# Performance work log

Measured on AMD Instinct MI355X. Metric: run time of the kernel, lower is better.

The kernel has to match this reference:

```python
import jax, jax.numpy as jnp
import numpy as np
import math

B, NX, NY = 4, 64, 64
IN_DIM, OUT_DIM = 3, 3
DIM, DEPTH, HEADS, DH, FF_MULT = 192, 6, 8, 64, 4
INNER = HEADS * DH              # 512
FF = DIM * FF_MULT              # 768
M = int(DH * math.log(DH))      # 266 random features (performer default)
GROUPS = 8
LATENT_STEPS = 1
EPS_SN, EPS_K, EPS_GN = 1e-5, 1e-4, 1e-5


def setup_inputs() -> dict:
    rng = np.random.default_rng(0)
    f = lambda *s: jnp.asarray(rng.standard_normal(s).astype(np.float32) * 0.02)
    # unitary forward operator (SVD-whitened in torch == orthogonal matrix)
    Q, _ = np.linalg.qr(rng.standard_normal((DIM, DIM)).astype(np.float32))
    return {
        "x": jnp.asarray(rng.standard_normal((B, NX, NY, IN_DIM)).astype(np.float32)),
        "to_in_w": f(DIM, IN_DIM), "to_in_b": f(DIM),
        "pos_emb": f(1, NX * NY, DIM),
        "proj": jnp.asarray(rng.standard_normal((DEPTH, M, DH)).astype(np.float32)),
        "sn_attn_g": jnp.ones((DEPTH,), jnp.float32),
        "wq": f(DEPTH, INNER, DIM), "wk": f(DEPTH, INNER, DIM), "wv": f(DEPTH, INNER, DIM),
        "wo": f(DEPTH, DIM, INNER), "bo": f(DEPTH, DIM),
        "sn_ff_g": jnp.ones((DEPTH,), jnp.float32),
        "w1": f(DEPTH, FF, DIM), "b1": f(DEPTH, FF),
        "w2": f(DEPTH, DIM, FF), "b2": f(DEPTH, DIM),
        "expand_w": f(DIM, DIM),
        "fwd_w": jnp.asarray(Q.astype(np.float32)),
        "dec_lin_w": f(DIM, DIM), "dec_lin_b": f(DIM),
        "gn_g": jnp.ones((DIM,), jnp.float32), "gn_b": jnp.zeros((DIM,), jnp.float32),
        "c9_w": f(DIM, DIM // GROUPS, 9, 9), "c9_b": f(DIM),
        "c7_w": f(DIM // 2, DIM // GROUPS, 7, 7), "c7_b": f(DIM // 2),
        "c5_w": f(DIM // 4, (DIM // 2) // GROUPS, 5, 5), "c5_b": f(DIM // 4),
        "c1_w": f(OUT_DIM, DIM // 4, 1, 1), "c1_b": f(OUT_DIM),
        "latent_steps": LATENT_STEPS,
    }


def _scalenorm(x, g):
    n = jnp.linalg.norm(x, axis=-1, keepdims=True) * (x.shape[-1] ** -0.5)
    return x / jnp.maximum(n, EPS_SN) * g


def _softmax_features(data, proj, is_query):
    # data: [b,h,n,d]; proj: [m,d] -> FAVOR+ softmax-kernel features [b,h,n,m]
    dn = data.shape[-1] ** -0.25
    ratio = proj.shape[0] ** -0.5
    dd = jnp.einsum('bhnd,md->bhnm', data * dn, proj)
    diag = 0.5 * jnp.sum(data * data, -1) * (dn * dn)  # [b,h,n]
    if is_query:
        mx = jnp.max(dd, axis=-1, keepdims=True)
    else:
        mx = jnp.max(dd, axis=(-1, -2), keepdims=True)
    return ratio * (jnp.exp(dd - diag[..., None] - mx) + EPS_K)


def _attn(x, proj, wq, wk, wv, wo, bo):
    b, n, _ = x.shape
    split = lambda t: t.reshape(b, n, HEADS, DH).transpose(0, 2, 1, 3)
    q = split(x @ wq.T); k = split(x @ wk.T); v = split(x @ wv.T)
    qp = _softmax_features(q, proj, True)
    kp = _softmax_features(k, proj, False)
    context = jnp.einsum('bhnm,bhnd->bhmd', kp, v)            # [b,h,m,d]
    denom = jnp.einsum('bhnm,bhm->bhn', qp, kp.sum(2))
    out = jnp.einsum('bhnm,bhmd->bhnd', qp, context) / denom[..., None]
    out = out.transpose(0, 2, 1, 3).reshape(b, n, INNER)
    return out @ wo.T + bo


def _circ_conv(x, w, b, groups):
    p = w.shape[-1] // 2
    x = jnp.pad(x, ((0, 0), (0, 0), (p, p), (p, p)), mode='wrap')
    y = jax.lax.conv_general_dilated(x, w, (1, 1), 'VALID',
        dimension_numbers=('NCHW', 'OIHW', 'NCHW'), feature_group_count=groups)
    return y + b[None, :, None, None]


def _group_norm(x, g, b):
    B_, C, H, W = x.shape
    xg = x.reshape(B_, GROUPS, C // GROUPS, H, W)
    mu = xg.mean((2, 3, 4), keepdims=True)
    var = xg.var((2, 3, 4), keepdims=True)
    xn = ((xg - mu) * jax.lax.rsqrt(var + EPS_GN)).reshape(B_, C, H, W)
    return xn * g[None, :, None, None] + b[None, :, None, None]


def reference(x, to_in_w, to_in_b, pos_emb, proj, sn_attn_g, wq, wk, wv, wo, bo,
              sn_ff_g, w1, b1, w2, b2, expand_w, fwd_w, dec_lin_w, dec_lin_b,
              gn_g, gn_b, c9_w, c9_b, c7_w, c7_b, c5_w, c5_b, c1_w, c1_b, latent_steps):
    b, nx, ny, _ = x.shape
    h = x @ to_in_w.T + to_in_b                       # [b,nx,ny,dim]
    h = h.reshape(b, nx * ny, DIM) + pos_emb[:, :nx * ny]
    for i in range(DEPTH):                             # Performer: prenorm attn + prenorm FF
        h = h + _attn(_scalenorm(h, sn_attn_g[i]), proj[i], wq[i], wk[i], wv[i], wo[i], bo[i])
        hn = _scalenorm(h, sn_ff_g[i])
        h = h + (jax.nn.gelu(hn @ w1[i].T + b1[i], approximate=False) @ w2[i].T + b2[i])
    h = h.reshape(b, nx, ny, DIM) @ expand_w.T        # expand_latent (no bias)
    u, us = h, []
    for _ in range(latent_steps):
        u = u @ fwd_w.T                               # unitary forward operator
        us.append(u)
    u = jnp.concatenate(us, 0)                        # [(b*t), nx, ny, c]
    y = u @ dec_lin_w.T + dec_lin_b
    y = y.transpose(0, 3, 1, 2)                       # NCHW
    y = _group_norm(y, gn_g, gn_b)
    y = jax.nn.gelu(_circ_conv(y, c9_w, c9_b, GROUPS), approximate=False)
    y = jax.nn.gelu(_circ_conv(y, c7_w, c7_b, GROUPS), approximate=False)
    y = jax.nn.gelu(_circ_conv(y, c5_w, c5_b, GROUPS), approximate=False)
    y = jax.lax.conv_general_dilated(y, c1_w, (1, 1), 'VALID',
        dimension_numbers=('NCHW', 'OIHW', 'NCHW')) + c1_b[None, :, None, None]
    # einops '(b t) c nx ny -> b t nx ny c'
    y = y.reshape(b, latent_steps, OUT_DIM, nx, ny).transpose(0, 1, 3, 4, 2)
    return y
```

## Files before the change

### kernel.cpp

```cpp
#include <hip/hip_runtime.h>
#include <cmath>

#define NB      4
#define NTOK    4096
#define BNTOK   16384
#define CDIM    192
#define CINNER  512
#define NHEADS  8
#define DHEAD   64
#define CFF     768
#define MFEAT   266
#define NDEPTH  6

#define DN      0.35355339059327373f
#define RATIO   0.06131393394849658f

typedef unsigned short u16;
typedef __attribute__((ext_vector_type(8))) short s16x8;
typedef __attribute__((ext_vector_type(8))) u16  u16x8;
typedef __attribute__((ext_vector_type(4))) float f32x4;

#define OFF_H    0ull
#define OFF_HN   3145728ull
#define OFF_Q    6291456ull
#define OFF_K    14680064ull
#define OFF_V    23068672ull
#define OFF_BIG  31457280ull
#define OFF_PJ   44040192ull
#define OFF_CTXT 44163072ull
#define OFF_KMAX 47368192ull
#define OFF_GNP  47368448ull
#define OFF_GNS  47369472ull
#define OFF_WHI  47370240ull
#define OFF_WLO  49489920ull
#define WOFF_QKV 0ull
#define WOFF_WO  1769472ull
#define WOFF_W1  2359296ull
#define WOFF_W2  3244032ull
#define WOFF_EXP 4128768ull
#define WOFF_FWD 4165632ull
#define WOFF_DEC 4202496ull

#define PJL      20480
#define CTXTN    819200

__device__ __forceinline__ float gelu_f(float x) {
    return 0.5f * x * (1.0f + erff(x * 0.7071067811865476f));
}
__device__ __forceinline__ unsigned f2ord(float f) {
    int i = __float_as_int(f);
    return (i >= 0) ? ((unsigned)i | 0x80000000u) : (unsigned)(~i);
}
__device__ __forceinline__ float ord2f(unsigned u) {
    int i = (u & 0x80000000u) ? (int)(u & 0x7fffffffu) : ~(int)u;
    return __int_as_float(i);
}
__device__ __forceinline__ void split_bf16(float a, u16& h, u16& l) {
    unsigned ua = __float_as_uint(a);
    unsigned rh = (ua + 0x7FFFu + ((ua >> 16) & 1u)) >> 16;
    h = (u16)rh;
    float hf = __uint_as_float(rh << 16);
    float lo = a - hf;
    unsigned ul = __float_as_uint(lo);
    unsigned rl = (ul + 0x7FFFu + ((ul >> 16) & 1u)) >> 16;
    l = (u16)rl;
}
__device__ __forceinline__ u16 hi_bf16(float a) {
    unsigned ua = __float_as_uint(a);
    return (u16)((ua + 0x7FFFu + ((ua >> 16) & 1u)) >> 16);
}

__global__ __launch_bounds__(256) void cvt_qkv(const float* __restrict__ wq,
    const float* __restrict__ wk, const float* __restrict__ wv,
    u16* __restrict__ hi, u16* __restrict__ lo)
{
    int idx = blockIdx.x * 256 + threadIdx.x;
    int l = idx / 294912, rem = idx - l * 294912;
    int r = rem / 192, c = rem - r * 192;
    float v;
    if (r < 512)       v = wq[((size_t)l * 512 + r) * 192 + c];
    else if (r < 1024) v = wk[((size_t)l * 512 + (r - 512)) * 192 + c];
    else               v = wv[((size_t)l * 512 + (r - 1024)) * 192 + c];
    u16 h, lw; split_bf16(v, h, lw);
    hi[idx] = h; lo[idx] = lw;
}

__global__ __launch_bounds__(256) void cvt_w(const float* __restrict__ src,
    u16* __restrict__ hi, u16* __restrict__ lo, int n)
{
    int idx = blockIdx.x * 256 + threadIdx.x;
    if (idx < n) {
        u16 h, l; split_bf16(src[idx], h, l);
        hi[idx] = h; lo[idx] = l;
    }
}

__global__ __launch_bounds__(256) void cvt_dec(const float* __restrict__ e,
    const float* __restrict__ f, const float* __restrict__ d,
    u16* __restrict__ hi, u16* __restrict__ lo)
{
    int idx = blockIdx.x * 256 + threadIdx.x;
    if (idx >= 110592) return;
    int which = idx / 36864, rem = idx - which * 36864;
    float v = (which == 0) ? e[rem] : (which == 1) ? f[rem] : d[rem];
    u16 h, l; split_bf16(v, h, l);
    hi[idx] = h; lo[idx] = l;
}

__global__ __launch_bounds__(256) void cvt_pj(const float* __restrict__ proj,
    u16* __restrict__ hi, u16* __restrict__ lo)
{
    int idx = blockIdx.x * 256 + threadIdx.x;
    int l = idx / PJL, rem = idx - l * PJL;
    int m = rem >> 6, k = rem & 63;
    float v = (m < MFEAT) ? proj[(size_t)l * MFEAT * DHEAD + m * 64 + k] : 0.f;
    u16 h, lw; split_bf16(v, h, lw);
    hi[idx] = h; lo[idx] = lw;
}

__global__ __launch_bounds__(256) void input_embed(const float* __restrict__ x,
    const float* __restrict__ w, const float* __restrict__ bvec,
    const float* __restrict__ pos, float* __restrict__ h)
{
    int idx = blockIdx.x * 256 + threadIdx.x;
    int row = idx / CDIM, c = idx - row * CDIM;
    int p = row & (NTOK - 1);
    const float* xr = x + (size_t)row * 3;
    h[idx] = xr[0]*w[c*3+0] + xr[1]*w[c*3+1] + xr[2]*w[c*3+2] + bvec[c] + pos[(size_t)p*CDIM + c];
}

__global__ __launch_bounds__(256) void scalenorm_kernel(const float* __restrict__ in,
    float* __restrict__ out, const float* __restrict__ gptr, int gidx)
{
    int wv = threadIdx.x >> 6, lane = threadIdx.x & 63;
    int row = blockIdx.x * 4 + wv;
    const float* p = in + (size_t)row * CDIM;
    float x0 = p[lane], x1 = p[lane + 64], x2 = p[lane + 128];
    float ss = x0*x0 + x1*x1 + x2*x2;
    #pragma unroll
    for (int off = 32; off; off >>= 1) ss += __shfl_xor(ss, off);
    float g = gptr[gidx];
    float n = sqrtf(ss * (1.0f / 192.0f));
    float s = g / fmaxf(n, 1e-5f);
    float* o = out + (size_t)row * CDIM;
    o[lane] = x0 * s; o[lane + 64] = x1 * s; o[lane + 128] = x2 * s;
}

#define LP 40
__global__ __launch_bounds__(256) void gemm_mfma(const float* __restrict__ A,
    const u16* __restrict__ Bhi, const u16* __restrict__ Blo,
    const float* __restrict__ bias, const float* __restrict__ resid,
    float* __restrict__ C, int M, int N, int K, int epi)
{
    __shared__ u16 a_hi[128 * LP], a_lo[128 * LP], b_hi[128 * LP], b_lo[128 * LP];
    const int tid = threadIdx.x;
    const int n0 = blockIdx.x * 128, m0 = blockIdx.y * 128;
    const int wave = tid >> 6, lane = tid & 63;
    const int wr = wave >> 1, wc = wave & 1;
    const int fr = lane & 15, q = lane >> 4;
    f32x4 acc[4][4];
    #pragma unroll
    for (int i = 0; i < 4; ++i)
        #pragma unroll
        for (int j = 0; j < 4; ++j) { acc[i][j][0]=0.f; acc[i][j][1]=0.f; acc[i][j][2]=0.f; acc[i][j][3]=0.f; }

    const int srow = tid >> 1, sc0 = (tid & 1) * 16;
    const float* aptr = A + (size_t)(m0 + srow) * K + sc0;
    const bool bval = (n0 + srow) < N;
    const u16* bhp = Bhi + (size_t)(n0 + srow) * K + sc0;
    const u16* blp = Blo + (size_t)(n0 + srow) * K + sc0;
    const int soff = srow * LP + sc0;
    const int aoffb = (wr * 64 + fr) * LP + q * 8;
    const int boffb = (wc * 64 + fr) * LP + q * 8;

    for (int kc = 0; kc < K; kc += 32) {
        float4 f0 = *(const float4*)(aptr + kc);
        float4 f1 = *(const float4*)(aptr + kc + 4);
        float4 f2 = *(const float4*)(aptr + kc + 8);
        float4 f3 = *(const float4*)(aptr + kc + 12);
        u16x8 h0, l0, h1, l1;
        {
            float v[16] = {f0.x,f0.y,f0.z,f0.w, f1.x,f1.y,f1.z,f1.w,
                           f2.x,f2.y,f2.z,f2.w, f3.x,f3.y,f3.z,f3.w};
            u16 hh[16], ll[16];
            #pragma unroll
            for (int i = 0; i < 16; ++i) split_bf16(v[i], hh[i], ll[i]);
            #pragma unroll
            for (int i = 0; i < 8; ++i) { h0[i]=hh[i]; l0[i]=ll[i]; h1[i]=hh[8+i]; l1[i]=ll[8+i]; }
        }
        *(u16x8*)&a_hi[soff]     = h0;  *(u16x8*)&a_hi[soff + 8] = h1;
        *(u16x8*)&a_lo[soff]     = l0;  *(u16x8*)&a_lo[soff + 8] = l1;
        u16x8 bh0 = (u16x8)0, bh1 = (u16x8)0, bl0 = (u16x8)0, bl1 = (u16x8)0;
        if (bval) {
            bh0 = *(const u16x8*)(bhp + kc);  bh1 = *(const u16x8*)(bhp + kc + 8);
            bl0 = *(const u16x8*)(blp + kc);  bl1 = *(const u16x8*)(blp + kc + 8);
        }
        *(u16x8*)&b_hi[soff]     = bh0;  *(u16x8*)&b_hi[soff + 8] = bh1;
        *(u16x8*)&b_lo[soff]     = bl0;  *(u16x8*)&b_lo[soff + 8] = bl1;
        __syncthreads();
        s16x8 Ah[4], Al[4], Bh[4], Bl[4];
        #pragma unroll
        for (int t = 0; t < 4; ++t) {
            Ah[t] = *(const s16x8*)&a_hi[aoffb + t * 16 * LP];
            Al[t] = *(const s16x8*)&a_lo[aoffb + t * 16 * LP];
            Bh[t] = *(const s16x8*)&b_hi[boffb + t * 16 * LP];
            Bl[t] = *(const s16x8*)&b_lo[boffb + t * 16 * LP];
        }
        #pragma unroll
        for (int i = 0; i < 4; ++i)
            #pragma unroll
            for (int j = 0; j < 4; ++j)
                acc[i][j] = __builtin_amdgcn_mfma_f32_16x16x32_bf16(Ah[i], Bh[j], acc[i][j], 0, 0, 0);
        #pragma unroll
        for (int i = 0; i < 4; ++i)
            #pragma unroll
            for (int j = 0; j < 4; ++j)
                acc[i][j] = __builtin_amdgcn_mfma_f32_16x16x32_bf16(Ah[i], Bl[j], acc[i][j], 0, 0, 0);
        #pragma unroll
        for (int i = 0; i < 4; ++i)
            #pragma unroll
            for (int j = 0; j < 4; ++j)
                acc[i][j] = __builtin_amdgcn_mfma_f32_16x16x32_bf16(Al[i], Bh[j], acc[i][j], 0, 0, 0);
        __syncthreads();
    }
    const int c0 = n0 + wc * 64;
    const int rowb = m0 + wr * 64;
    #pragma unroll
    for (int j = 0; j < 4; ++j) {
        int c = c0 + j * 16 + fr;
        if (c >= N) continue;
        float bb = (epi & 1) ? bias[c] : 0.f;
        float* cp;
        if (epi & 8) cp = C + (size_t)(c >> 9) * 8388608ull + (size_t)(c & 511);
        else         cp = C + c;
        const float* rp = (epi & 4) ? (resid + c) : nullptr;
        #pragma unroll
        for (int i = 0; i < 4; ++i) {
            #pragma unroll
            for (int r = 0; r < 4; ++r) {
                int row = rowb + i * 16 + q * 4 + r;
                float val = acc[i][j][r] + bb;
                if (epi & 2) val = gelu_f(val);
                if (epi & 4) val += rp[(size_t)row * N];
                size_t off = (epi & 8) ? (size_t)row * 512 : (size_t)row * N;
                cp[off] = val;
            }
        }
    }
}

__global__ void kmax_init(unsigned* kmaxu) {
    if (threadIdx.x < NDEPTH * 32) kmaxu[threadIdx.x] = 0u;
}

__global__ __launch_bounds__(256) void kmax2_kernel(const float* __restrict__ Km,
    const u16* __restrict__ pjh, unsigned* __restrict__ kmaxu)
{
    __shared__ __align__(16) u16 khi[64 * 72];
    __shared__ float wred[4];
    const int tid = threadIdx.x;
    const int nt = blockIdx.x, bh = blockIdx.y;
    const int b = bh >> 3, hh = bh & 7;
    const int wave = tid >> 6, lane = tid & 63;
    const int fr = lane & 15, quad = lane >> 4;
    float lm = -1e30f;
    const size_t kbase = ((size_t)b * NTOK) * CINNER + hh * DHEAD;
    for (int ch = 0; ch < 8; ++ch) {
        const int n0 = nt * 512 + ch * 64;
        __syncthreads();
        {
            int tok = tid >> 2, koff = (tid & 3) * 16;
            const float* kp = Km + kbase + (size_t)(n0 + tok) * CINNER + koff;
            u16 hh16[16];
            #pragma unroll
            for (int qd = 0; qd < 4; ++qd) {
                float4 f = *(const float4*)(kp + qd * 4);
                hh16[qd*4+0] = hi_bf16(f.x * DN); hh16[qd*4+1] = hi_bf16(f.y * DN);
                hh16[qd*4+2] = hi_bf16(f.z * DN); hh16[qd*4+3] = hi_bf16(f.w * DN);
            }
            u16x8 v0, v1;
            #pragma unroll
            for (int i = 0; i < 8; ++i) { v0[i] = hh16[i]; v1[i] = hh16[8+i]; }
            *(u16x8*)&khi[tok * 72 + koff] = v0;
            *(u16x8*)&khi[tok * 72 + koff + 8] = v1;
        }
        __syncthreads();
        int rowA = (wave * 16 + fr) * 72;
        s16x8 A0 = *(const s16x8*)&khi[rowA + quad * 8];
        s16x8 A1 = *(const s16x8*)&khi[rowA + 32 + quad * 8];
        for (int ct = 0; ct < 17; ++ct) {
            const u16* bp = pjh + (ct * 16 + fr) * 64 + quad * 8;
            s16x8 B0 = *(const s16x8*)bp;
            s16x8 B1 = *(const s16x8*)(bp + 32);
            f32x4 t; t[0]=0.f; t[1]=0.f; t[2]=0.f; t[3]=0.f;
            t = __builtin_amdgcn_mfma_f32_16x16x32_bf16(A0, B0, t, 0, 0, 0);
            t = __builtin_amdgcn_mfma_f32_16x16x32_bf16(A1, B1, t, 0, 0, 0);
            if (ct * 16 + fr < MFEAT) {
                #pragma unroll
                for (int r = 0; r < 4; ++r) lm = fmaxf(lm, t[r]);
            }
        }
    }
    #pragma unroll
    for (int off = 32; off; off >>= 1) lm = fmaxf(lm, __shfl_xor(lm, off));
    if (lane == 0) wred[wave] = lm;
    __syncthreads();
    if (tid == 0) {
        float m = fmaxf(fmaxf(wred[0], wred[1]), fmaxf(wred[2], wred[3]));
        atomicMax(kmaxu + bh, f2ord(m));
    }
}

__global__ __launch_bounds__(256) void ctx2_kernel(const float* __restrict__ Km,
    const float* __restrict__ Vm, const u16* __restrict__ pjh, const u16* __restrict__ pjl,
    const unsigned* __restrict__ kmaxu, float* __restrict__ part)
{
    __shared__ __align__(16) u16 khi[32 * 72], klo[32 * 72];
    __shared__ __align__(16) u16 vth[80 * 40], vtl[80 * 40];
    __shared__ __align__(16) u16 kph[64 * 40], kpl[64 * 40];
    __shared__ float diag[32];
    const int tid = threadIdx.x;
    const int bh = blockIdx.x, seg = blockIdx.y;
    const int b = bh >> 3, hh = bh & 7;
    const int wave = tid >> 6, lane = tid & 63;
    const int fr = lane & 15, quad = lane >> 4;
    const float kmx = ord2f(kmaxu[bh]);
    for (int i = tid; i < 16 * 40; i += 256) {
        int row = 64 + i / 40, col = i - (i / 40) * 40;
        vth[row * 40 + col] = (row == 64) ? (u16)0x3F80 : (u16)0;
        vtl[row * 40 + col] = 0;
    }
    f32x4 accv[5][5];
    #pragma unroll
    for (int i = 0; i < 5; ++i)
        #pragma unroll
        for (int j = 0; j < 5; ++j) { accv[i][j][0]=0.f; accv[i][j][1]=0.f; accv[i][j][2]=0.f; accv[i][j][3]=0.f; }
    const size_t rowbase = ((size_t)b * NTOK) * CINNER + hh * DHEAD;
    const int rt = wave & 1, ctp = wave >> 1;
    for (int nc = 0; nc < 16; ++nc) {
        const int n0 = seg * 512 + nc * 32;
        __syncthreads();
        {
            int tok = tid >> 3, koff = (tid & 7) * 8;
            const float* kp = Km + rowbase + (size_t)(n0 + tok) * CINNER + koff;
            float4 f0 = *(const float4*)kp;
            float4 f1 = *(const float4*)(kp + 4);
            float v[8] = {f0.x*DN, f0.y*DN, f0.z*DN, f0.w*DN, f1.x*DN, f1.y*DN, f1.z*DN, f1.w*DN};
            u16x8 hv, lv; float ps = 0.f;
            #pragma unroll
            for (int i = 0; i < 8; ++i) { u16 h, l; split_bf16(v[i], h, l); hv[i]=h; lv[i]=l; ps += v[i]*v[i]; }
            *(u16x8*)&khi[tok * 72 + koff] = hv;
            *(u16x8*)&klo[tok * 72 + koff] = lv;
            ps += __shfl_xor(ps, 1); ps += __shfl_xor(ps, 2); ps += __shfl_xor(ps, 4);
            if ((tid & 7) == 0) diag[tok] = 0.5f * ps;
            const float* vp = Vm + rowbase + (size_t)(n0 + tok) * CINNER + koff;
            float4 g0 = *(const float4*)vp;
            float4 g1 = *(const float4*)(vp + 4);
            float vv[8] = {g0.x, g0.y, g0.z, g0.w, g1.x, g1.y, g1.z, g1.w};
            #pragma unroll
            for (int i = 0; i < 8; ++i) {
                u16 h, l; split_bf16(vv[i], h, l);
                vth[(koff + i) * 40 + tok] = h;
                vtl[(koff + i) * 40 + tok] = l;
            }
        }
        __syncthreads();
        for (int mc = 0; mc < 5; ++mc) {
            f32x4 dd2[2];
            dd2[0][0]=0.f; dd2[0][1]=0.f; dd2[0][2]=0.f; dd2[0][3]=0.f;
            dd2[1] = dd2[0];
            {
                int rowA = (rt * 16 + fr) * 72;
                s16x8 A0h = *(const s16x8*)&khi[rowA + quad * 8];
                s16x8 A1h = *(const s16x8*)&khi[rowA + 32 + quad * 8];
                s16x8 A0l = *(const s16x8*)&klo[rowA + quad * 8];
                s16x8 A1l = *(const s16x8*)&klo[rowA + 32 + quad * 8];
                #pragma unroll
                for (int c = 0; c < 2; ++c) {
                    int ct = mc * 4 + ctp * 2 + c;
                    const u16* bph = pjh + (ct * 16 + fr) * 64 + quad * 8;
                    const u16* bpl = pjl + (ct * 16 + fr) * 64 + quad * 8;
                    s16x8 B0h = *(const s16x8*)bph, B1h = *(const s16x8*)(bph + 32);
                    s16x8 B0l = *(const s16x8*)bpl, B1l = *(const s16x8*)(bpl + 32);
                    dd2[c] = __builtin_amdgcn_mfma_f32_16x16x32_bf16(A0h, B0h, dd2[c], 0, 0, 0);
                    dd2[c] = __builtin_amdgcn_mfma_f32_16x16x32_bf16(A0h, B0l, dd2[c], 0, 0, 0);
                    dd2[c] = __builtin_amdgcn_mfma_f32_16x16x32_bf16(A0l, B0h, dd2[c], 0, 0, 0);
                    dd2[c] = __builtin_amdgcn_mfma_f32_16x16x32_bf16(A1h, B1h, dd2[c], 0, 0, 0);
                    dd2[c] = __builtin_amdgcn_mfma_f32_16x16x32_bf16(A1h, B1l, dd2[c], 0, 0, 0);
                    dd2[c] = __builtin_amdgcn_mfma_f32_16x16x32_bf16(A1l, B1h, dd2[c], 0, 0, 0);
                }
            }
            #pragma unroll
            for (int c = 0; c < 2; ++c) {
                int ct = mc * 4 + ctp * 2 + c;
                bool valid = (ct * 16 + fr) < MFEAT;
                ushort4 ph, pl;
                #pragma unroll
                for (int r = 0; r < 4; ++r) {
                    float dgv = diag[rt * 16 + quad * 4 + r];
                    float val = valid ? RATIO * (expf(dd2[c][r] - dgv - kmx) + 1e-4f) : 0.f;
                    u16 h, l; split_bf16(val, h, l);
                    (&ph.x)[r] = h; (&pl.x)[r] = l;
                }
                int ml = (ctp * 2 + c) * 16 + fr;
                *(ushort4*)&kph[ml * 40 + rt * 16 + quad * 4] = ph;
                *(ushort4*)&kpl[ml * 40 + rt * 16 + quad * 4] = pl;
            }
            __syncthreads();
            {
                s16x8 Bh = *(const s16x8*)&kph[(wave * 16 + fr) * 40 + quad * 8];
                s16x8 Bl = *(const s16x8*)&kpl[(wave * 16 + fr) * 40 + quad * 8];
                #pragma unroll
                for (int rt2 = 0; rt2 < 5; ++rt2) {
                    s16x8 Ah = *(const s16x8*)&vth[(rt2 * 16 + fr) * 40 + quad * 8];
                    s16x8 Al = *(const s16x8*)&vtl[(rt2 * 16 + fr) * 40 + quad * 8];
                    accv[rt2][mc] = __builtin_amdgcn_mfma_f32_16x16x32_bf16(Ah, Bh, accv[rt2][mc], 0, 0, 0);
                    accv[rt2][mc] = __builtin_amdgcn_mfma_f32_16x16x32_bf16(Ah, Bl, accv[rt2][mc], 0, 0, 0);
                    accv[rt2][mc] = __builtin_amdgcn_mfma_f32_16x16x32_bf16(Al, Bh, accv[rt2][mc], 0, 0, 0);
                }
            }
            __syncthreads();
        }
    }
    float* pb = part + ((size_t)(seg * 32 + bh)) * 80 * 320;
    #pragma unroll
    for (int rt2 = 0; rt2 < 5; ++rt2) {
        #pragma unroll
        for (int mc = 0; mc < 5; ++mc) {
            int ct = mc * 4 + wave;
            #pragma unroll
            for (int r = 0; r < 4; ++r)
                pb[(size_t)(rt2 * 16 + quad * 4 + r) * 320 + ct * 16 + fr] = accv[rt2][mc][r];
        }
    }
}

__global__ __launch_bounds__(256) void ctxt_reduce(const float* __restrict__ part,
    u16* __restrict__ cth, u16* __restrict__ ctl)
{
    int idx = blockIdx.x * 256 + threadIdx.x;
    float s = 0.f;
    #pragma unroll
    for (int sg = 0; sg < 8; ++sg) s += part[(size_t)sg * CTXTN + idx];
    u16 h, l; split_bf16(s, h, l);
    cth[idx] = h; ctl[idx] = l;
}

__global__ __launch_bounds__(256) void qside2_kernel(const float* __restrict__ Qm,
    const u16* __restrict__ pjh, const u16* __restrict__ pjl,
    const u16* __restrict__ cth, const u16* __restrict__ ctl,
    float* __restrict__ attn_out)
{
    __shared__ __align__(16) u16 qhi[64 * 72], qlo[64 * 72];
    __shared__ __align__(16) u16 slabh[4][16 * 72], slabl[4][16 * 72];
    __shared__ float diag[64];
    const int tid = threadIdx.x;
    const int nt = blockIdx.x, bh = blockIdx.y;
    const int b = bh >> 3, hh = bh & 7;
    const int wave = tid >> 6, lane = tid & 63;
    const int fr = lane & 15, quad = lane >> 4;
    const int n0 = nt * 64;
    {
        int tok = tid >> 2, koff = (tid & 3) * 16;
        const float* qp = Qm + ((size_t)(b * NTOK + n0 + tok)) * CINNER + hh * DHEAD + koff;
        float v[16]; float ps = 0.f;
        #pragma unroll
        for (int qd = 0; qd < 4; ++qd) {
            float4 f = *(const float4*)(qp + qd * 4);
            v[qd*4+0]=f.x*DN; v[qd*4+1]=f.y*DN; v[qd*4+2]=f.z*DN; v[qd*4+3]=f.w*DN;
        }
        u16x8 h0, l0, h1, l1;
        #pragma unroll
        for (int i = 0; i < 8; ++i) {
            u16 h, l; split_bf16(v[i], h, l); h0[i]=h; l0[i]=l;
            split_bf16(v[8+i], h, l); h1[i]=h; l1[i]=l;
        }
        #pragma unroll
        for (int i = 0; i < 16; ++i) ps += v[i]*v[i];
        *(u16x8*)&qhi[tok * 72 + koff] = h0;  *(u16x8*)&qhi[tok * 72 + koff + 8] = h1;
        *(u16x8*)&qlo[tok * 72 + koff] = l0;  *(u16x8*)&qlo[tok * 72 + koff + 8] = l1;
        ps += __shfl_xor(ps, 1); ps += __shfl_xor(ps, 2);
        if ((tid & 3) == 0) diag[tok] = 0.5f * ps;
    }
    __syncthreads();
    f32x4 dd[20];
    #pragma unroll
    for (int ct = 0; ct < 20; ++ct) { dd[ct][0]=0.f; dd[ct][1]=0.f; dd[ct][2]=0.f; dd[ct][3]=0.f; }
    {
        int rowA = (wave * 16 + fr) * 72;
        s16x8 A0h = *(const s16x8*)&qhi[rowA + quad * 8];
        s16x8 A1h = *(const s16x8*)&qhi[rowA + 32 + quad * 8];
        s16x8 A0l = *(const s16x8*)&qlo[rowA + quad * 8];
        s16x8 A1l = *(const s16x8*)&qlo[rowA + 32 + quad * 8];
        #pragma unroll
        for (int ct = 0; ct < 20; ++ct) {
            const u16* bph = pjh + (ct * 16 + fr) * 64 + quad * 8;
            const u16* bpl = pjl + (ct * 16 + fr) * 64 + quad * 8;
            s16x8 B0h = *(const s16x8*)bph, B1h = *(const s16x8*)(bph + 32);
            s16x8 B0l = *(const s16x8*)bpl, B1l = *(const s16x8*)(bpl + 32);
            dd[ct] = __builtin_amdgcn_mfma_f32_16x16x32_bf16(A0h, B0h, dd[ct], 0, 0, 0);
            dd[ct] = __builtin_amdgcn_mfma_f32_16x16x32_bf16(A0h, B0l, dd[ct], 0, 0, 0);
            dd[ct] = __builtin_amdgcn_mfma_f32_16x16x32_bf16(A0l, B0h, dd[ct], 0, 0, 0);
            dd[ct] = __builtin_amdgcn_mfma_f32_16x16x32_bf16(A1h, B1h, dd[ct], 0, 0, 0);
            dd[ct] = __builtin_amdgcn_mfma_f32_16x16x32_bf16(A1h, B1l, dd[ct], 0, 0, 0);
            dd[ct] = __builtin_amdgcn_mfma_f32_16x16x32_bf16(A1l, B1h, dd[ct], 0, 0, 0);
        }
    }
    float pm[4] = {-1e30f, -1e30f, -1e30f, -1e30f};
    #pragma unroll
    for (int ct = 0; ct < 20; ++ct) {
        if (ct * 16 + fr < MFEAT) {
            #pragma unroll
            for (int r = 0; r < 4; ++r) pm[r] = fmaxf(pm[r], dd[ct][r]);
        }
    }
    #pragma unroll
    for (int r = 0; r < 4; ++r) {
        pm[r] = fmaxf(pm[r], __shfl_xor(pm[r], 1));
        pm[r] = fmaxf(pm[r], __shfl_xor(pm[r], 2));
        pm[r] = fmaxf(pm[r], __shfl_xor(pm[r], 4));
        pm[r] = fmaxf(pm[r], __shfl_xor(pm[r], 8));
    }
    float dg[4];
    #pragma unroll
    for (int r = 0; r < 4; ++r) dg[r] = diag[wave * 16 + quad * 4 + r];
    #pragma unroll
    for (int ct = 0; ct < 20; ++ct) {
        bool valid = (ct * 16 + fr) < MFEAT;
        #pragma unroll
        for (int r = 0; r < 4; ++r)
            dd[ct][r] = valid ? RATIO * (expf(dd[ct][r] - dg[r] - pm[r]) + 1e-4f) : 0.f;
    }
    f32x4 acc[5];
    #pragma unroll
    for (int dt = 0; dt < 5; ++dt) { acc[dt][0]=0.f; acc[dt][1]=0.f; acc[dt][2]=0.f; acc[dt][3]=0.f; }
    u16* sh = slabh[wave];  u16* sl = slabl[wave];
    for (int mc = 0; mc < 5; ++mc) {
        #pragma unroll
        for (int c = 0; c < 4; ++c) {
            int ct = mc * 4 + c;
            #pragma unroll
            for (int r = 0; r < 4; ++r) {
                u16 h, l; split_bf16(dd[ct][r], h, l);
                int tok = quad * 4 + r;
                sh[tok * 72 + c * 16 + fr] = h;
                sl[tok * 72 + c * 16 + fr] = l;
            }
        }
        __syncthreads();
        #pragma unroll
        for (int ks = 0; ks < 2; ++ks) {
            s16x8 Ah = *(const s16x8*)&sh[fr * 72 + ks * 32 + quad * 8];
            s16x8 Al = *(const s16x8*)&sl[fr * 72 + ks * 32 + quad * 8];
            #pragma unroll
            for (int dt = 0; dt < 5; ++dt) {
                const u16* bph = cth + ((size_t)bh * 80 + dt * 16 + fr) * 320 + mc * 64 + ks * 32 + quad * 8;
                const u16* bpl = ctl + ((size_t)bh * 80 + dt * 16 + fr) * 320 + mc * 64 + ks * 32 + quad * 8;
                s16x8 Bh = *(const s16x8*)bph;
                s16x8 Bl = *(const s16x8*)bpl;
                acc[dt] = __builtin_amdgcn_mfma_f32_16x16x32_bf16(Ah, Bh, acc[dt], 0, 0, 0);
                acc[dt] = __builtin_amdgcn_mfma_f32_16x16x32_bf16(Ah, Bl, acc[dt], 0, 0, 0);
                acc[dt] = __builtin_amdgcn_mfma_f32_16x16x32_bf16(Al, Bh, acc[dt], 0, 0, 0);
            }
        }
        __syncthreads();
    }
    #pragma unroll
    for (int r = 0; r < 4; ++r) {
        float denom = __shfl(acc[4][r], lane & 48);
        float inv = 1.0f / denom;
        int token = n0 + wave * 16 + quad * 4 + r;
        float* op = attn_out + ((size_t)(b * NTOK + token)) * CINNER + hh * DHEAD;
        #pragma unroll
        for (int dt = 0; dt < 4; ++dt)
            op[dt * 16 + fr] = acc[dt][r] * inv;
    }
}

__global__ __launch_bounds__(256) void gn_part_kernel(const float* __restrict__ y,
    float2* __restrict__ part)
{
    __shared__ float s_s[256], s_q[256];
    const int tid = threadIdx.x;
    const int sp = blockIdx.x, g = blockIdx.y, b = blockIdx.z;
    int p = sp * 256 + tid;
    const float* base = y + ((size_t)(b * NTOK + p)) * CDIM + g * 24;
    float s = 0.f, q = 0.f;
    #pragma unroll
    for (int i = 0; i < 24; ++i) { float v = base[i]; s += v; q += v * v; }
    s_s[tid] = s; s_q[tid] = q;
    __syncthreads();
    for (int st = 128; st; st >>= 1) {
        if (tid < st) { s_s[tid] += s_s[tid + st]; s_q[tid] += s_q[tid + st]; }
        __syncthreads();
    }
    if (tid == 0) part[(b * 8 + g) * 16 + sp] = make_float2(s_s[0], s_q[0]);
}

__global__ void gn_stat_kernel(const float2* __restrict__ part, float2* __restrict__ stat)
{
    int bg = threadIdx.x;
    if (bg < 32) {
        float s = 0.f, q = 0.f;
        for (int i = 0; i < 16; ++i) { float2 v = part[bg * 16 + i]; s += v.x; q += v.y; }
        float mean = s * (1.0f / 98304.0f);
        float var = q * (1.0f / 98304.0f) - mean * mean;
        stat[bg] = make_float2(mean, rsqrtf(var + 1e-5f));
    }
}

__global__ __launch_bounds__(256) void gn_apply_kernel(const float* __restrict__ y,
    const float2* __restrict__ stat, const float* __restrict__ gg,
    const float* __restrict__ gb, float* __restrict__ out)
{
    __shared__ float tile[64][65];
    const int tid = threadIdx.x;
    const int pt = blockIdx.x, ct = blockIdx.y, b = blockIdx.z;
    const int p0 = pt * 64, c0 = ct * 64;
    #pragma unroll
    for (int r = 0; r < 4; ++r) {
        int id = tid + r * 256;
        int pr = id >> 4, kq = (id & 15) * 4;
        float4 v = *(const float4*)(y + ((size_t)(b * NTOK + p0 + pr)) * CDIM + c0 + kq);
        tile[pr][kq+0] = v.x; tile[pr][kq+1] = v.y; tile[pr][kq+2] = v.z; tile[pr][kq+3] = v.w;
    }
    __syncthreads();
    const int cc = tid >> 6, pp = tid & 63;
    #pragma unroll
    for (int i = 0; i < 16; ++i) {
        int c = c0 + cc * 16 + i;
        int g = c / 24;
        float2 st = stat[b * 8 + g];
        float v = tile[pp][cc * 16 + i];
        out[((size_t)(b * CDIM + c)) * NTOK + p0 + pp] = (v - st.x) * st.y * gg[c] + gb[c];
    }
}

template<int KS, int CIN, int COUT, int OX, int YS, int OCB>
__global__ __launch_bounds__(256) void circ_conv2(const float* __restrict__ in,
    const float* __restrict__ w, const float* __restrict__ bias,
    float* __restrict__ out, int do_gelu)
{
    constexpr int P   = KS / 2;
    constexpr int ICG = CIN / 8;
    constexpr int OCG = COUT / 8;
    constexpr int TW  = 64 + 2 * P;
    constexpr int TR  = 64 / YS + 2 * P;
    constexpr int RS0 = (TW + 3) & ~3;
    constexpr int RS  = (RS0 % 8 == 0) ? RS0 + 4 : RS0;
    constexpr int TCX = 64 / OX;
    constexpr int RV  = (OX + KS - 1 + 3) & ~3;
    __shared__ __align__(16) float tile[TR * RS];
    const int tid = threadIdx.x;
    const int oc0 = blockIdx.x * OCB;
    const int y0  = blockIdx.y * (64 / YS);
    const int b   = blockIdx.z;
    const int g   = oc0 / OCG;
    const int tx  = tid % TCX, ty = tid / TCX;
    float acc[OCB][OX] = {};
    const float* ip0 = in + ((size_t)(b * CIN + g * ICG)) * 4096;
    #pragma unroll 1
    for (int ic = 0; ic < ICG; ++ic) {
        __syncthreads();
        const float* ip = ip0 + (size_t)ic * 4096;
        for (int idx = tid; idx < TR * TW; idx += 256) {
            int r = idx / TW, c = idx - r * TW;
            int gy = (y0 + r - P) & 63, gx = (c - P) & 63;
            tile[r * RS + c] = ip[gy * 64 + gx];
        }
        __syncthreads();
        const float* wp = w + ((size_t)oc0 * ICG + ic) * (KS * KS);
        #pragma unroll 1
        for (int ky = 0; ky < KS; ++ky) {
            float wreg[OCB][KS];
            #pragma unroll
            for (int oc = 0; oc < OCB; ++oc)
                #pragma unroll
                for (int kx = 0; kx < KS; ++kx)
                    wreg[oc][kx] = wp[(size_t)oc * ICG * KS * KS + ky * KS + kx];
            float rv[RV];
            const float* rp = &tile[(ty + ky) * RS + tx * OX];
            #pragma unroll
            for (int q2 = 0; q2 < RV / 4; ++q2)
                *(float4*)&rv[q2 * 4] = *(const float4*)(rp + q2 * 4);
            #pragma unroll
            for (int kx = 0; kx < KS; ++kx)
                #pragma unroll
                for (int oc = 0; oc < OCB; ++oc)
                    #pragma unroll
                    for (int ox = 0; ox < OX; ++ox)
                        acc[oc][ox] += rv[kx + ox] * wreg[oc][kx];
        }
    }
    const int y = y0 + ty, x = tx * OX;
    #pragma unroll
    for (int oc = 0; oc < OCB; ++oc) {
        float bv = bias[oc0 + oc];
        float vo[OX];
        #pragma unroll
        for (int ox = 0; ox < OX; ++ox) {
            float vv = acc[oc][ox] + bv;
            vo[ox] = do_gelu ? gelu_f(vv) : vv;
        }
        float* op = out + (((size_t)(b * COUT + oc0 + oc) * 64 + y)) * 64 + x;
        #pragma unroll
        for (int q2 = 0; q2 < OX / 4; ++q2)
            *(float4*)(op + q2 * 4) = *(float4*)&vo[q2 * 4];
    }
}

__global__ __launch_bounds__(256) void conv1_kernel(const float* __restrict__ in,
    const float* __restrict__ w, const float* __restrict__ bias, float* __restrict__ out)
{
    int idx = blockIdx.x * 256 + threadIdx.x;
    int b = idx >> 12, p = idx & 4095;
    float a0 = bias[0], a1 = bias[1], a2 = bias[2];
    const float* ip = in + (size_t)b * 48 * NTOK + p;
    #pragma unroll 8
    for (int ic = 0; ic < 48; ++ic) {
        float v = ip[(size_t)ic * NTOK];
        a0 += v * w[ic]; a1 += v * w[48 + ic]; a2 += v * w[96 + ic];
    }
    float* op = out + (size_t)idx * 3;
    op[0] = a0; op[1] = a1; op[2] = a2;
}

static inline void gemm_mf(hipStream_t s, const float* A, const u16* Bhi, const u16* Blo,
                           const float* bias, const float* resid, float* C,
                           int M, int N, int K, int epi)
{
    dim3 g((N + 127) / 128, M / 128);
    hipLaunchKernelGGL(gemm_mfma, g, dim3(256), 0, s, A, Bhi, Blo, bias, resid, C, M, N, K, epi);
}

extern "C" void kernel_launch(void* const* d_in, const int* in_sizes, int n_in,
                              void* d_out, int out_size, void* d_ws, size_t ws_size,
                              hipStream_t stream)
{
    (void)in_sizes; (void)n_in; (void)out_size; (void)ws_size;
    const float* x        = (const float*)d_in[0];
    const float* to_in_w  = (const float*)d_in[1];
    const float* to_in_b  = (const float*)d_in[2];
    const float* pos_emb  = (const float*)d_in[3];
    const float* proj     = (const float*)d_in[4];
    const float* sn_attn_g= (const float*)d_in[5];
    const float* wq       = (const float*)d_in[6];
    const float* wk       = (const float*)d_in[7];
    const float* wv       = (const float*)d_in[8];
    const float* wo       = (const float*)d_in[9];
    const float* bo       = (const float*)d_in[10];
    const float* sn_ff_g  = (const float*)d_in[11];
    const float* w1       = (const float*)d_in[12];
    const float* b1       = (const float*)d_in[13];
    const float* w2       = (const float*)d_in[14];
    const float* b2       = (const float*)d_in[15];
    const float* expand_w = (const float*)d_in[16];
    const float* fwd_w    = (const float*)d_in[17];
    const float* dec_lin_w= (const float*)d_in[18];
    const float* dec_lin_b= (const float*)d_in[19];
    const float* gn_g     = (const float*)d_in[20];
    const float* gn_b     = (const float*)d_in[21];
    const float* c9_w     = (const float*)d_in[22];
    const float* c9_b     = (const float*)d_in[23];
    const float* c7_w     = (const float*)d_in[24];
    const float* c7_b     = (const float*)d_in[25];
    const float* c5_w     = (const float*)d_in[26];
    const float* c5_b     = (const float*)d_in[27];
    const float* c1_w     = (const float*)d_in[28];
    const float* c1_b     = (const float*)d_in[29];
    float* out = (float*)d_out;

    float* ws = (float*)d_ws;
    float* h   = ws + OFF_H;
    float* hn  = ws + OFF_HN;
    float* q   = ws + OFF_Q;
    float* k   = ws + OFF_K;
    float* v   = ws + OFF_V;
    float* big = ws + OFF_BIG;
    u16* pjhi = (u16*)(ws + OFF_PJ);
    u16* pjlo = pjhi + 6 * PJL;
    u16* cthi = (u16*)(ws + OFF_CTXT);
    u16* ctlo = cthi + CTXTN;
    unsigned* kmaxu = (unsigned*)(ws + OFF_KMAX);
    float2* gnp = (float2*)(ws + OFF_GNP);
    float2* gns = (float2*)(ws + OFF_GNS);
    u16* whi = (u16*)(ws + OFF_WHI);
    u16* wlo = (u16*)(ws + OFF_WLO);

    hipLaunchKernelGGL(input_embed, dim3(BNTOK * CDIM / 256), dim3(256), 0, stream,
                       x, to_in_w, to_in_b, pos_emb, h);
    hipLaunchKernelGGL(kmax_init, dim3(1), dim3(256), 0, stream, kmaxu);
    hipLaunchKernelGGL(cvt_qkv, dim3(6912), dim3(256), 0, stream, wq, wk, wv,
                       whi + WOFF_QKV, wlo + WOFF_QKV);
    hipLaunchKernelGGL(cvt_w, dim3(2304), dim3(256), 0, stream, wo, whi + WOFF_WO, wlo + WOFF_WO, 589824);
    hipLaunchKernelGGL(cvt_w, dim3(3456), dim3(256), 0, stream, w1, whi + WOFF_W1, wlo + WOFF_W1, 884736);
    hipLaunchKernelGGL(cvt_w, dim3(3456), dim3(256), 0, stream, w2, whi + WOFF_W2, wlo + WOFF_W2, 884736);
    hipLaunchKernelGGL(cvt_dec, dim3(432), dim3(256), 0, stream, expand_w, fwd_w, dec_lin_w,
                       whi + WOFF_EXP, wlo + WOFF_EXP);
    hipLaunchKernelGGL(cvt_pj, dim3(480), dim3(256), 0, stream, proj, pjhi, pjlo);

    for (int l = 0; l < NDEPTH; ++l) {
        const float* bo_l = bo + (size_t)l * CDIM;
        const float* b1_l = b1 + (size_t)l * CFF;
        const float* b2_l = b2 + (size_t)l * CDIM;
        const u16* pjh_l = pjhi + (size_t)l * PJL;
        const u16* pjl_l = pjlo + (size_t)l * PJL;
        unsigned* kmax_l = kmaxu + l * 32;

        hipLaunchKernelGGL(scalenorm_kernel, dim3(BNTOK / 4), dim3(256), 0, stream, h, hn, sn_attn_g, l);
        gemm_mf(stream, hn, whi + WOFF_QKV + (size_t)l * 294912, wlo + WOFF_QKV + (size_t)l * 294912,
                nullptr, nullptr, q, BNTOK, 1536, CDIM, 8);
        hipLaunchKernelGGL(kmax2_kernel, dim3(8, 32), dim3(256), 0, stream, k, pjh_l, kmax_l);
        hipLaunchKernelGGL(ctx2_kernel, dim3(32, 8), dim3(256), 0, stream, k, v, pjh_l, pjl_l, kmax_l, big);
        hipLaunchKernelGGL(ctxt_reduce, dim3(CTXTN / 256), dim3(256), 0, stream, big, cthi, ctlo);
        hipLaunchKernelGGL(qside2_kernel, dim3(64, 32), dim3(256), 0, stream, q, pjh_l, pjl_l, cthi, ctlo, k);
        gemm_mf(stream, k, whi + WOFF_WO + (size_t)l * 98304, wlo + WOFF_WO + (size_t)l * 98304,
                bo_l, h, h, BNTOK, CDIM, CINNER, 1 | 4);

        hipLaunchKernelGGL(scalenorm_kernel, dim3(BNTOK / 4), dim3(256), 0, stream, h, hn, sn_ff_g, l);
        gemm_mf(stream, hn, whi + WOFF_W1 + (size_t)l * 147456, wlo + WOFF_W1 + (size_t)l * 147456,
                b1_l, nullptr, big, BNTOK, CFF, CDIM, 1 | 2);
        gemm_mf(stream, big, whi + WOFF_W2 + (size_t)l * 147456, wlo + WOFF_W2 + (size_t)l * 147456,
                b2_l, h, h, BNTOK, CDIM, CFF, 1 | 4);
    }

    gemm_mf(stream, h, whi + WOFF_EXP, wlo + WOFF_EXP, nullptr, nullptr, hn, BNTOK, CDIM, CDIM, 0);
    gemm_mf(stream, hn, whi + WOFF_FWD, wlo + WOFF_FWD, nullptr, nullptr, h, BNTOK, CDIM, CDIM, 0);
    gemm_mf(stream, h, whi + WOFF_DEC, wlo + WOFF_DEC, dec_lin_b, nullptr, hn, BNTOK, CDIM, CDIM, 1);

    float* y0 = big;
    float* y1 = big + 3145728;
    float* y2 = big + 6291456;
    float* y3 = big + 7864320;
    hipLaunchKernelGGL(gn_part_kernel, dim3(16, 8, 4), dim3(256), 0, stream, hn, gnp);
    hipLaunchKernelGGL(gn_stat_kernel, dim3(1), dim3(32), 0, stream, gnp, gns);
    hipLaunchKernelGGL(gn_apply_kernel, dim3(64, 3, 4), dim3(256), 0, stream, hn, gns, gn_g, gn_b, y0);

    hipLaunchKernelGGL((circ_conv2<9, 192, 192, 8, 2, 2>), dim3(96, 2, 4), dim3(256), 0, stream,
                       y0, c9_w, c9_b, y1, 1);
    hipLaunchKernelGGL((circ_conv2<7, 192, 96, 8, 2, 2>), dim3(48, 2, 4), dim3(256), 0, stream,
                       y1, c7_w, c7_b, y2, 1);
    hipLaunchKernelGGL((circ_conv2<5, 96, 48, 4, 4, 2>), dim3(24, 4, 4), dim3(256), 0, stream,
                       y2, c5_w, c5_b, y3, 1);
    hipLaunchKernelGGL(conv1_kernel, dim3(BNTOK / 256), dim3(256), 0, stream, y3, c1_w, c1_b, out);
}
```

Measured before the change: 3.780 ms.

## Skip idle GEMM waves, per-wave ctx features, more kmax/conv blocks

In the GEMM, waves whose column tile lies past N skip the MFMA work entirely. ctx2 is restructured so each wave computes its own feature tile into private shared memory, which removes two block barriers per feature chunk. kmax gets twice as many blocks, each handling half the tokens, and the 9x9 and 7x7 circular convs are retiled to launch more blocks. qside2 drops its per-chunk barriers, which risks a race if its shared buffer is shared across waves.

```diff
diff --git a/kernel.cpp b/kernel.cpp
--- a/kernel.cpp
+++ b/kernel.cpp
@@ -158,6 +158,7 @@
     const int wave = tid >> 6, lane = tid & 63;
     const int wr = wave >> 1, wc = wave & 1;
     const int fr = lane & 15, q = lane >> 4;
+    const bool wactive = (n0 + wc * 64) < N;
     f32x4 acc[4][4];
     #pragma unroll
     for (int i = 0; i < 4; ++i)
@@ -198,29 +199,31 @@
         *(u16x8*)&b_hi[soff]     = bh0;  *(u16x8*)&b_hi[soff + 8] = bh1;
         *(u16x8*)&b_lo[soff]     = bl0;  *(u16x8*)&b_lo[soff + 8] = bl1;
         __syncthreads();
-        s16x8 Ah[4], Al[4], Bh[4], Bl[4];
-        #pragma unroll
-        for (int t = 0; t < 4; ++t) {
-            Ah[t] = *(const s16x8*)&a_hi[aoffb + t * 16 * LP];
-            Al[t] = *(const s16x8*)&a_lo[aoffb + t * 16 * LP];
-            Bh[t] = *(const s16x8*)&b_hi[boffb + t * 16 * LP];
-            Bl[t] = *(const s16x8*)&b_lo[boffb + t * 16 * LP];
-        }
-        #pragma unroll
-        for (int i = 0; i < 4; ++i)
-            #pragma unroll
-            for (int j = 0; j < 4; ++j)
-                acc[i][j] = __builtin_amdgcn_mfma_f32_16x16x32_bf16(Ah[i], Bh[j], acc[i][j], 0, 0, 0);
-        #pragma unroll
-        for (int i = 0; i < 4; ++i)
-            #pragma unroll
-            for (int j = 0; j < 4; ++j)
-                acc[i][j] = __builtin_amdgcn_mfma_f32_16x16x32_bf16(Ah[i], Bl[j], acc[i][j], 0, 0, 0);
-        #pragma unroll
-        for (int i = 0; i < 4; ++i)
-            #pragma unroll
-            for (int j = 0; j < 4; ++j)
-                acc[i][j] = __builtin_amdgcn_mfma_f32_16x16x32_bf16(Al[i], Bh[j], acc[i][j], 0, 0, 0);
+        if (wactive) {
+            s16x8 Ah[4], Al[4], Bh[4], Bl[4];
+            #pragma unroll
+            for (int t = 0; t < 4; ++t) {
+                Ah[t] = *(const s16x8*)&a_hi[aoffb + t * 16 * LP];
+                Al[t] = *(const s16x8*)&a_lo[aoffb + t * 16 * LP];
+                Bh[t] = *(const s16x8*)&b_hi[boffb + t * 16 * LP];
+                Bl[t] = *(const s16x8*)&b_lo[boffb + t * 16 * LP];
+            }
+            #pragma unroll
+            for (int i = 0; i < 4; ++i)
+                #pragma unroll
+                for (int j = 0; j < 4; ++j)
+                    acc[i][j] = __builtin_amdgcn_mfma_f32_16x16x32_bf16(Ah[i], Bh[j], acc[i][j], 0, 0, 0);
+            #pragma unroll
+            for (int i = 0; i < 4; ++i)
+                #pragma unroll
+                for (int j = 0; j < 4; ++j)
+                    acc[i][j] = __builtin_amdgcn_mfma_f32_16x16x32_bf16(Ah[i], Bl[j], acc[i][j], 0, 0, 0);
+            #pragma unroll
+            for (int i = 0; i < 4; ++i)
+                #pragma unroll
+                for (int j = 0; j < 4; ++j)
+                    acc[i][j] = __builtin_amdgcn_mfma_f32_16x16x32_bf16(Al[i], Bh[j], acc[i][j], 0, 0, 0);
+        }
         __syncthreads();
     }
     const int c0 = n0 + wc * 64;
@@ -265,8 +268,8 @@
     const int fr = lane & 15, quad = lane >> 4;
     float lm = -1e30f;
     const size_t kbase = ((size_t)b * NTOK) * CINNER + hh * DHEAD;
-    for (int ch = 0; ch < 8; ++ch) {
-        const int n0 = nt * 512 + ch * 64;
+    for (int ch = 0; ch < 4; ++ch) {
+        const int n0 = nt * 256 + ch * 64;
         __syncthreads();
         {
             int tok = tid >> 2, koff = (tid & 3) * 16;
@@ -317,7 +320,7 @@
 {
     __shared__ __align__(16) u16 khi[32 * 72], klo[32 * 72];
     __shared__ __align__(16) u16 vth[80 * 40], vtl[80 * 40];
-    __shared__ __align__(16) u16 kph[64 * 40], kpl[64 * 40];
+    __shared__ __align__(16) u16 kph[4][16 * 40], kpl[4][16 * 40];
     __shared__ float diag[32];
     const int tid = threadIdx.x;
     const int bh = blockIdx.x, seg = blockIdx.y;
@@ -336,7 +339,7 @@
         #pragma unroll
         for (int j = 0; j < 5; ++j) { accv[i][j][0]=0.f; accv[i][j][1]=0.f; accv[i][j][2]=0.f; accv[i][j][3]=0.f; }
     const size_t rowbase = ((size_t)b * NTOK) * CINNER + hh * DHEAD;
-    const int rt = wave & 1, ctp = wave >> 1;
+    u16* sh = kph[wave];  u16* sl = kpl[wave];
     for (int nc = 0; nc < 16; ++nc) {
         const int n0 = seg * 512 + nc * 32;
         __syncthreads();
@@ -365,61 +368,52 @@
             }
         }
         __syncthreads();
+        s16x8 Ah[2][2], Al[2][2];
+        #pragma unroll
+        for (int rt = 0; rt < 2; ++rt) {
+            int rowA = (rt * 16 + fr) * 72;
+            Ah[rt][0] = *(const s16x8*)&khi[rowA + quad * 8];
+            Ah[rt][1] = *(const s16x8*)&khi[rowA + 32 + quad * 8];
+            Al[rt][0] = *(const s16x8*)&klo[rowA + quad * 8];
+            Al[rt][1] = *(const s16x8*)&klo[rowA + 32 + quad * 8];
+        }
         for (int mc = 0; mc < 5; ++mc) {
-            f32x4 dd2[2];
-            dd2[0][0]=0.f; dd2[0][1]=0.f; dd2[0][2]=0.f; dd2[0][3]=0.f;
-            dd2[1] = dd2[0];
-            {
-                int rowA = (rt * 16 + fr) * 72;
-                s16x8 A0h = *(const s16x8*)&khi[rowA + quad * 8];
-                s16x8 A1h = *(const s16x8*)&khi[rowA + 32 + quad * 8];
-                s16x8 A0l = *(const s16x8*)&klo[rowA + quad * 8];
-                s16x8 A1l = *(const s16x8*)&klo[rowA + 32 + quad * 8];
-                #pragma unroll
-                for (int c = 0; c < 2; ++c) {
-                    int ct = mc * 4 + ctp * 2 + c;
-                    const u16* bph = pjh + (ct * 16 + fr) * 64 + quad * 8;
-                    const u16* bpl = pjl + (ct * 16 + fr) * 64 + quad * 8;
-                    s16x8 B0h = *(const s16x8*)bph, B1h = *(const s16x8*)(bph + 32);
-                    s16x8 B0l = *(const s16x8*)bpl, B1l = *(const s16x8*)(bpl + 32);
-                    dd2[c] = __builtin_amdgcn_mfma_f32_16x16x32_bf16(A0h, B0h, dd2[c], 0, 0, 0);
-                    dd2[c] = __builtin_amdgcn_mfma_f32_16x16x32_bf16(A0h, B0l, dd2[c], 0, 0, 0);
-                    dd2[c] = __builtin_amdgcn_mfma_f32_16x16x32_bf16(A0l, B0h, dd2[c], 0, 0, 0);
-                    dd2[c] = __builtin_amdgcn_mfma_f32_16x16x32_bf16(A1h, B1h, dd2[c], 0, 0, 0);
-                    dd2[c] = __builtin_amdgcn_mfma_f32_16x16x32_bf16(A1h, B1l, dd2[c], 0, 0, 0);
-                    dd2[c] = __builtin_amdgcn_mfma_f32_16x16x32_bf16(A1l, B1h, dd2[c], 0, 0, 0);
-                }
-            }
-            #pragma unroll
-            for (int c = 0; c < 2; ++c) {
-                int ct = mc * 4 + ctp * 2 + c;
-                bool valid = (ct * 16 + fr) < MFEAT;
+            const int ct = mc * 4 + wave;
+            const u16* bph = pjh + (ct * 16 + fr) * 64 + quad * 8;
+            const u16* bpl = pjl + (ct * 16 + fr) * 64 + quad * 8;
+            s16x8 B0h = *(const s16x8*)bph, B1h = *(const s16x8*)(bph + 32);
+            s16x8 B0l = *(const s16x8*)bpl, B1l = *(const s16x8*)(bpl + 32);
+            const bool valid = (ct * 16 + fr) < MFEAT;
+            #pragma unroll
+            for (int rt = 0; rt < 2; ++rt) {
+                f32x4 dd; dd[0]=0.f; dd[1]=0.f; dd[2]=0.f; dd[3]=0.f;
+                dd = __builtin_amdgcn_mfma_f32_16x16x32_bf16(Ah[rt][0], B0h, dd, 0, 0, 0);
+                dd = __builtin_amdgcn_mfma_f32_16x16x32_bf16(Ah[rt][0], B0l, dd, 0, 0, 0);
+                dd = __builtin_amdgcn_mfma_f32_16x16x32_bf16(Al[rt][0], B0h, dd, 0, 0, 0);
+                dd = __builtin_amdgcn_mfma_f32_16x16x32_bf16(Ah[rt][1], B1h, dd, 0, 0, 0);
+                dd = __builtin_amdgcn_mfma_f32_16x16x32_bf16(Ah[rt][1], B1l, dd, 0, 0, 0);
+                dd = __builtin_amdgcn_mfma_f32_16x16x32_bf16(Al[rt][1], B1h, dd, 0, 0, 0);
                 ushort4 ph, pl;
                 #pragma unroll
                 for (int r = 0; r < 4; ++r) {
                     float dgv = diag[rt * 16 + quad * 4 + r];
-                    float val = valid ? RATIO * (expf(dd2[c][r] - dgv - kmx) + 1e-4f) : 0.f;
+                    float val = valid ? RATIO * (expf(dd[r] - dgv - kmx) + 1e-4f) : 0.f;
                     u16 h, l; split_bf16(val, h, l);
                     (&ph.x)[r] = h; (&pl.x)[r] = l;
                 }
-                int ml = (ctp * 2 + c) * 16 + fr;
-                *(ushort4*)&kph[ml * 40 + rt * 16 + quad * 4] = ph;
-                *(ushort4*)&kpl[ml * 40 + rt * 16 + quad * 4] = pl;
+                *(ushort4*)&sh[fr * 40 + rt * 16 + quad * 4] = ph;
+                *(ushort4*)&sl[fr * 40 + rt * 16 + quad * 4] = pl;
             }
-            __syncthreads();
-            {
-                s16x8 Bh = *(const s16x8*)&kph[(wave * 16 + fr) * 40 + quad * 8];
-                s16x8 Bl = *(const s16x8*)&kpl[(wave * 16 + fr) * 40 + quad * 8];
-                #pragma unroll
-                for (int rt2 = 0; rt2 < 5; ++rt2) {
-                    s16x8 Ah = *(const s16x8*)&vth[(rt2 * 16 + fr) * 40 + quad * 8];
-                    s16x8 Al = *(const s16x8*)&vtl[(rt2 * 16 + fr) * 40 + quad * 8];
-                    accv[rt2][mc] = __builtin_amdgcn_mfma_f32_16x16x32_bf16(Ah, Bh, accv[rt2][mc], 0, 0, 0);
-                    accv[rt2][mc] = __builtin_amdgcn_mfma_f32_16x16x32_bf16(Ah, Bl, accv[rt2][mc], 0, 0, 0);
-                    accv[rt2][mc] = __builtin_amdgcn_mfma_f32_16x16x32_bf16(Al, Bh, accv[rt2][mc], 0, 0, 0);
-                }
+            s16x8 Bh = *(const s16x8*)&sh[fr * 40 + quad * 8];
+            s16x8 Bl = *(const s16x8*)&sl[fr * 40 + quad * 8];
+            #pragma unroll
+            for (int rt2 = 0; rt2 < 5; ++rt2) {
+                s16x8 Vh = *(const s16x8*)&vth[(rt2 * 16 + fr) * 40 + quad * 8];
+                s16x8 Vl = *(const s16x8*)&vtl[(rt2 * 16 + fr) * 40 + quad * 8];
+                accv[rt2][mc] = __builtin_amdgcn_mfma_f32_16x16x32_bf16(Vh, Bh, accv[rt2][mc], 0, 0, 0);
+                accv[rt2][mc] = __builtin_amdgcn_mfma_f32_16x16x32_bf16(Vh, Bl, accv[rt2][mc], 0, 0, 0);
+                accv[rt2][mc] = __builtin_amdgcn_mfma_f32_16x16x32_bf16(Vl, Bh, accv[rt2][mc], 0, 0, 0);
             }
-            __syncthreads();
         }
     }
     float* pb = part + ((size_t)(seg * 32 + bh)) * 80 * 320;
@@ -547,7 +541,6 @@
                 sl[tok * 72 + c * 16 + fr] = l;
             }
         }
-        __syncthreads();
         #pragma unroll
         for (int ks = 0; ks < 2; ++ks) {
             s16x8 Ah = *(const s16x8*)&sh[fr * 72 + ks * 32 + quad * 8];
@@ -563,7 +556,6 @@
                 acc[dt] = __builtin_amdgcn_mfma_f32_16x16x32_bf16(Al, Bh, acc[dt], 0, 0, 0);
             }
         }
-        __syncthreads();
     }
     #pragma unroll
     for (int r = 0; r < 4; ++r) {
@@ -810,7 +802,7 @@
         hipLaunchKernelGGL(scalenorm_kernel, dim3(BNTOK / 4), dim3(256), 0, stream, h, hn, sn_attn_g, l);
         gemm_mf(stream, hn, whi + WOFF_QKV + (size_t)l * 294912, wlo + WOFF_QKV + (size_t)l * 294912,
                 nullptr, nullptr, q, BNTOK, 1536, CDIM, 8);
-        hipLaunchKernelGGL(kmax2_kernel, dim3(8, 32), dim3(256), 0, stream, k, pjh_l, kmax_l);
+        hipLaunchKernelGGL(kmax2_kernel, dim3(16, 32), dim3(256), 0, stream, k, pjh_l, kmax_l);
         hipLaunchKernelGGL(ctx2_kernel, dim3(32, 8), dim3(256), 0, stream, k, v, pjh_l, pjl_l, kmax_l, big);
         hipLaunchKernelGGL(ctxt_reduce, dim3(CTXTN / 256), dim3(256), 0, stream, big, cthi, ctlo);
         hipLaunchKernelGGL(qside2_kernel, dim3(64, 32), dim3(256), 0, stream, q, pjh_l, pjl_l, cthi, ctlo, k);
@@ -836,9 +828,9 @@
     hipLaunchKernelGGL(gn_stat_kernel, dim3(1), dim3(32), 0, stream, gnp, gns);
     hipLaunchKernelGGL(gn_apply_kernel, dim3(64, 3, 4), dim3(256), 0, stream, hn, gns, gn_g, gn_b, y0);
 
-    hipLaunchKernelGGL((circ_conv2<9, 192, 192, 8, 2, 2>), dim3(96, 2, 4), dim3(256), 0, stream,
+    hipLaunchKernelGGL((circ_conv2<9, 192, 192, 4, 4, 2>), dim3(96, 4, 4), dim3(256), 0, stream,
                        y0, c9_w, c9_b, y1, 1);
-    hipLaunchKernelGGL((circ_conv2<7, 192, 96, 8, 2, 2>), dim3(48, 2, 4), dim3(256), 0, stream,
+    hipLaunchKernelGGL((circ_conv2<7, 192, 96, 4, 4, 2>), dim3(48, 4, 4), dim3(256), 0, stream,
                        y1, c7_w, c7_b, y2, 1);
     hipLaunchKernelGGL((circ_conv2<5, 96, 48, 4, 4, 2>), dim3(24, 4, 4), dim3(256), 0, stream,
                        y2, c5_w, c5_b, y3, 1);
```

Result: faster. 3.634 ms (-3.9%).
